# Kernel optimization log

Hardware: AMD Instinct MI355X
Metric: run time of the kernel (lower is better)

Reference implementation:

```python
import jax, jax.numpy as jnp
import numpy as np

M_POS = 0.5
M_NEG_SIM = 0.1
LAM_NEG = 1.0


def setup_inputs() -> dict:
    key = jax.random.key(0)
    N, d, G = 8192, 1024, 64
    codebook = jax.random.normal(key, (N, d), dtype=jnp.float32)
    base = (jnp.arange(N) // G) * G  # contiguous groups of size G (vq_to_range)
    starts = base.astype(jnp.int32)
    ends = (base + G - 1).astype(jnp.int32)
    return {"codebook": codebook, "starts": starts, "ends": ends, "max_i": N - 1}


def reference(codebook, starts, ends, max_i):
    N, d = codebook.shape
    M = min(N, int(max_i) + 1)  # rows processed by the python loop

    # cosine similarity rows [0:M] vs all N
    zn = codebook / jnp.linalg.norm(codebook, axis=-1, keepdims=True)
    cos = jnp.einsum('md,nd->mn', zn[:M], zn)  # (M, N)

    # pairwise Euclidean distances rows [0:M] vs all N via ||a-b||^2 = |a|^2+|b|^2-2ab
    sq = jnp.sum(codebook * codebook, axis=-1)  # (N,)
    dot = jnp.einsum('md,nd->mn', codebook[:M], codebook)  # (M, N)
    d2 = jnp.maximum(sq[:M, None] + sq[None, :] - 2.0 * dot, 0.0)

    j = jnp.arange(N)[None, :]
    i = jnp.arange(M)[:, None]
    in_range = (j >= starts[:M, None]) & (j <= ends[:M, None])
    pos_mask = in_range & (j != i)
    # original: group_mask[i]=False then neg = ~group_mask, so i is in negatives
    neg_mask = (~in_range) | (j == i)

    pos_cnt = jnp.sum(pos_mask, axis=-1)
    neg_cnt = jnp.sum(neg_mask, axis=-1)

    # safe sqrt: only evaluate on positive-mask entries
    D = jnp.sqrt(jnp.where(pos_mask, d2, 1.0))
    pos_term = jnp.square(jax.nn.relu(D - M_POS)) * pos_mask
    pos_pull = jnp.sum(pos_term, axis=-1) / jnp.maximum(pos_cnt, 1)

    neg_cos = jnp.clip(cos, -1.0, 1.0)
    neg_term = jnp.square(jax.nn.relu(jnp.abs(neg_cos) - M_NEG_SIM)) * neg_mask
    ortho = jnp.sum(neg_term, axis=-1) / jnp.maximum(neg_cnt, 1)

    valid = (pos_cnt > 0) & (neg_cnt > 0)
    per_row = jnp.where(valid, pos_pull + LAM_NEG * ortho, 0.0)
    cnt = jnp.sum(valid)
    total = jnp.sum(per_row)
    return jnp.where(cnt > 0, total / jnp.maximum(cnt, 1).astype(total.dtype), jnp.zeros((), total.dtype))
```

## Files before the change

kernel.cpp:

```cpp
#include <hip/hip_runtime.h>
#include <hip/hip_bf16.h>
#include <stdint.h>

#define M_POS 0.5f
#define M_NEG 0.1f
#define LAM_NEG 1.0f

typedef __attribute__((ext_vector_type(4))) float floatx4;
using f8x8 = long;

__global__ __launch_bounds__(256) void prep_kernel(
    const float* __restrict__ cb, unsigned char* __restrict__ cb_q,
    float* __restrict__ sq, float* __restrict__ inv_norm,
    unsigned* __restrict__ zero_base, int zero_len,
    int N, int d)
{
    const int gi = blockIdx.x * 256 + threadIdx.x;
    if (gi < zero_len) zero_base[gi] = 0u;

    const int row = blockIdx.x;
    const float* src = cb + (size_t)row * d;
    unsigned char* dst = cb_q + (size_t)row * d;
    const int t = threadIdx.x;

    float s = 0.f;
    for (int c = t * 4; c < d; c += 1024) {
        float4 v = *(const float4*)(src + c);
        s += v.x * v.x + v.y * v.y + v.z * v.z + v.w * v.w;
        int pk = __builtin_amdgcn_cvt_pk_fp8_f32(v.x, v.y, 0, false);
        pk     = __builtin_amdgcn_cvt_pk_fp8_f32(v.z, v.w, pk, true);
        *(int*)(dst + c) = pk;
    }
    for (int o = 32; o > 0; o >>= 1) s += __shfl_down(s, o, 64);
    __shared__ float wsum[4];
    if ((t & 63) == 0) wsum[t >> 6] = s;
    __syncthreads();
    if (t == 0) {
        float tot = wsum[0] + wsum[1] + wsum[2] + wsum[3];
        sq[row] = tot;
        inv_norm[row] = rsqrtf(tot);
    }
}

__global__ __launch_bounds__(256) void gram_loss_kernel(
    const unsigned char* __restrict__ A,
    const float* __restrict__ sq, const float* __restrict__ inv_norm,
    const int* __restrict__ starts, const int* __restrict__ ends,
    const int* __restrict__ max_ip,
    float* __restrict__ pos_acc, float* __restrict__ neg_acc,
    int N, int d)
{
    const int M = min(N, max_ip[0] + 1);

    const int t = blockIdx.x;
    int bx = (int)((sqrtf(8.f * (float)t + 1.f) - 1.f) * 0.5f);
    while ((bx + 1) * (bx + 2) / 2 <= t) bx++;
    while (bx * (bx + 1) / 2 > t) bx--;
    const int by = t - bx * (bx + 1) / 2;

    const int rowBase = by * 128;
    const int colBase = bx * 128;
    const bool isDiag = (by == bx);

    __shared__ alignas(16) unsigned char ldsA[128 * 64];
    __shared__ alignas(16) unsigned char ldsB[128 * 64];

    const int tid  = threadIdx.x;
    const int wave = tid >> 6;
    const int lane = tid & 63;
    const int wr = (wave >> 1) * 64;
    const int wc = (wave & 1) * 64;

    floatx4 acc[4][4];
#pragma unroll
    for (int a = 0; a < 4; ++a)
#pragma unroll
        for (int b = 0; b < 4; ++b) acc[a][b] = (floatx4){0.f, 0.f, 0.f, 0.f};

    const int sR = lane >> 2;
    const int sQ = lane & 3;
    const int kTiles = d / 64;

    const int rl = lane & 15;
    const int g  = lane >> 4;
    const int rowx = (rl >> 1) & 3;
    const int ghalf = g >> 1;
    const int godd  = (g & 1) * 8;

    for (int kt = 0; kt < kTiles; ++kt) {
        __syncthreads();
        const int k0 = kt * 64;
#pragma unroll
        for (int h = 0; h < 2; ++h) {
            const int r = wave * 32 + h * 16 + sR;
            const int srcQ = sQ ^ ((r >> 1) & 3);
            const unsigned char* ga = A + (size_t)(rowBase + r) * d + k0 + srcQ * 16;
            const unsigned char* gb = A + (size_t)(colBase + r) * d + k0 + srcQ * 16;
            __builtin_amdgcn_global_load_lds(
                (const __attribute__((address_space(1))) void*)ga,
                (__attribute__((address_space(3))) void*)(ldsA + r * 64 + sQ * 16), 16, 0, 0);
            __builtin_amdgcn_global_load_lds(
                (const __attribute__((address_space(1))) void*)gb,
                (__attribute__((address_space(3))) void*)(ldsB + r * 64 + sQ * 16), 16, 0, 0);
        }
        __syncthreads();

#pragma unroll
        for (int ko = 0; ko < 2; ++ko) {
            const int phys16 = ((ko * 2 + ghalf) ^ rowx);
            const int koff = phys16 * 16 + godd;
            f8x8 af[4], bf[4];
#pragma unroll
            for (int t4 = 0; t4 < 4; ++t4) {
                const int ra = wr + t4 * 16 + rl;
                const int rb = wc + t4 * 16 + rl;
                af[t4] = *(const f8x8*)(ldsA + ra * 64 + koff);
                bf[t4] = *(const f8x8*)(ldsB + rb * 64 + koff);
            }
#pragma unroll
            for (int rt = 0; rt < 4; ++rt)
#pragma unroll
                for (int ct = 0; ct < 4; ++ct)
                    acc[rt][ct] = __builtin_amdgcn_mfma_f32_16x16x32_fp8_fp8(
                        af[rt], bf[ct], acc[rt][ct], 0, 0, 0);
        }
    }

    const int q  = lane >> 4;
    const int jlo = colBase + wc;
    const int ilo = rowBase + wr;

    int   jn[4];
    float jinv[4];
    bool  jvalid[4];
#pragma unroll
    for (int ct = 0; ct < 4; ++ct) {
        const int j = jlo + ct * 16 + rl;
        jn[ct]  = j;
        jinv[ct] = inv_norm[j];
        jvalid[ct] = (j < M);
    }

    bool posLane = false;
    {
        const int ri = ilo + lane;
        if (ri < M) posLane |= (ends[ri] >= jlo) && (starts[ri] <= jlo + 63);
        if (!isDiag) {
            const int cj = jlo + lane;
            if (cj < M) posLane |= (ends[cj] >= ilo) && (starts[cj] <= ilo + 63);
        }
    }
    const bool fullPath = (__ballot(posLane) != 0ULL);

    float posc[4] = {0.f, 0.f, 0.f, 0.f};
    float negc[4] = {0.f, 0.f, 0.f, 0.f};

    if (fullPath) {
        int   jns[4], jne[4];
        float jsq[4];
#pragma unroll
        for (int ct = 0; ct < 4; ++ct) {
            jsq[ct] = sq[jn[ct]];
            jns[ct] = jvalid[ct] ? starts[jn[ct]] : 0;
            jne[ct] = jvalid[ct] ? ends[jn[ct]]   : -1;
        }
#pragma unroll
        for (int rt = 0; rt < 4; ++rt) {
            const int ibase = rowBase + wr + rt * 16 + q * 4;
#pragma unroll
            for (int reg = 0; reg < 4; ++reg) {
                const int i = ibase + reg;
                const bool rowValid = (i < M);
                const int ns = rowValid ? starts[i] : 0;
                const int ne = rowValid ? ends[i]   : -1;
                const float iinv = inv_norm[i];
                const float isq  = sq[i];
                float posp = 0.f, negp = 0.f;
#pragma unroll
                for (int ct = 0; ct < 4; ++ct) {
                    const float dot = acc[rt][ct][reg];
                    const int j = jn[ct];
                    float cosv = dot * iinv * jinv[ct];
                    cosv = fminf(fmaxf(cosv, -1.f), 1.f);
                    float tn = fmaxf(fabsf(cosv) - M_NEG, 0.f);
                    const float nterm = tn * tn;
                    const float d2 = fmaxf(isq + jsq[ct] - 2.f * dot, 0.f);
                    float tp = fmaxf(sqrtf(d2) - M_POS, 0.f);
                    const float pterm = tp * tp;
                    const bool dg = (j == i);
                    if (rowValid) {
                        const bool in_r = (j >= ns) && (j <= ne);
                        if (in_r && !dg) posp += pterm;
                        if (!in_r || dg) negp += nterm;
                    }
                    if (!isDiag && jvalid[ct]) {
                        const bool in_c = (i >= jns[ct]) && (i <= jne[ct]);
                        if (in_c && !dg) posc[ct] += pterm;
                        if (!in_c || dg) negc[ct] += nterm;
                    }
                }
#pragma unroll
                for (int m = 1; m < 16; m <<= 1) {
                    posp += __shfl_xor(posp, m, 64);
                    negp += __shfl_xor(negp, m, 64);
                }
                if (rowValid && rl == 0) {
                    atomicAdd(&pos_acc[i], posp);
                    atomicAdd(&neg_acc[i], negp);
                }
            }
        }
        if (!isDiag) {
#pragma unroll
            for (int ct = 0; ct < 4; ++ct) {
                posc[ct] += __shfl_xor(posc[ct], 16, 64);
                posc[ct] += __shfl_xor(posc[ct], 32, 64);
                negc[ct] += __shfl_xor(negc[ct], 16, 64);
                negc[ct] += __shfl_xor(negc[ct], 32, 64);
            }
            if (q == 0) {
#pragma unroll
                for (int ct = 0; ct < 4; ++ct) {
                    if (jvalid[ct]) {
                        atomicAdd(&pos_acc[jn[ct]], posc[ct]);
                        atomicAdd(&neg_acc[jn[ct]], negc[ct]);
                    }
                }
            }
        }
    } else {
#pragma unroll
        for (int rt = 0; rt < 4; ++rt) {
            const int ibase = rowBase + wr + rt * 16 + q * 4;
#pragma unroll
            for (int reg = 0; reg < 4; ++reg) {
                const int i = ibase + reg;
                const float iinv = inv_norm[i];
                float negp = 0.f;
#pragma unroll
                for (int ct = 0; ct < 4; ++ct) {
                    const float dot = acc[rt][ct][reg];
                    float cosv = dot * iinv * jinv[ct];
                    cosv = fminf(fmaxf(cosv, -1.f), 1.f);
                    float tn = fmaxf(fabsf(cosv) - M_NEG, 0.f);
                    const float nterm = tn * tn;
                    negp += nterm;
                    negc[ct] += nterm;
                }
#pragma unroll
                for (int m = 1; m < 16; m <<= 1)
                    negp += __shfl_xor(negp, m, 64);
                if ((i < M) && rl == 0)
                    atomicAdd(&neg_acc[i], negp);
            }
        }
        if (!isDiag) {
#pragma unroll
            for (int ct = 0; ct < 4; ++ct) {
                negc[ct] += __shfl_xor(negc[ct], 16, 64);
                negc[ct] += __shfl_xor(negc[ct], 32, 64);
            }
            if (q == 0) {
#pragma unroll
                for (int ct = 0; ct < 4; ++ct)
                    if (jvalid[ct])
                        atomicAdd(&neg_acc[jn[ct]], negc[ct]);
            }
        }
    }
}

__global__ __launch_bounds__(1024) void finalize_kernel(
    const float* __restrict__ pos_acc, const float* __restrict__ neg_acc,
    const int* __restrict__ starts, const int* __restrict__ ends,
    const int* __restrict__ max_ip, int N, float* __restrict__ out)
{
    const int M = min(N, max_ip[0] + 1);
    const int t = threadIdx.x;
    float total = 0.f;
    int cnt = 0;
    for (int i = t; i < M; i += blockDim.x) {
        const int ns = starts[i], ne = ends[i];
        const int lo = max(ns, 0), hi = min(ne, N - 1);
        const int inr = max(hi - lo + 1, 0);
        const bool dg = (i >= ns) && (i <= ne);
        const int pos_cnt = inr - (dg ? 1 : 0);
        const int neg_cnt = N - inr + (dg ? 1 : 0);
        if (pos_cnt > 0 && neg_cnt > 0) {
            total += pos_acc[i] / (float)max(pos_cnt, 1)
                   + LAM_NEG * neg_acc[i] / (float)max(neg_cnt, 1);
            cnt++;
        }
    }
    for (int o = 32; o > 0; o >>= 1) {
        total += __shfl_down(total, o, 64);
        cnt   += __shfl_down(cnt, o, 64);
    }
    __shared__ float ts[16];
    __shared__ int   cs[16];
    const int w = t >> 6;
    if ((t & 63) == 0) { ts[w] = total; cs[w] = cnt; }
    __syncthreads();
    if (t == 0) {
        float T = 0.f; int C = 0;
        const int nw = blockDim.x >> 6;
        for (int i = 0; i < nw; ++i) { T += ts[i]; C += cs[i]; }
        out[0] = (C > 0) ? T / (float)C : 0.f;
    }
}

extern "C" void kernel_launch(void* const* d_in, const int* in_sizes, int n_in,
                              void* d_out, int out_size, void* d_ws, size_t ws_size,
                              hipStream_t stream) {
    const float* cb     = (const float*)d_in[0];
    const int*   starts = (const int*)d_in[1];
    const int*   ends   = (const int*)d_in[2];
    const int*   max_ip = (const int*)d_in[3];
    float* out = (float*)d_out;

    const int N = in_sizes[1];
    const int d = in_sizes[0] / N;

    char* ws = (char*)d_ws;
    unsigned char* cb_q = (unsigned char*)ws;
    size_t off = ((size_t)N * d + 255) & ~(size_t)255;
    float* sq       = (float*)(ws + off); off += (size_t)N * 4;
    float* inv_norm = (float*)(ws + off); off += (size_t)N * 4;
    float* pos_acc  = (float*)(ws + off); off += (size_t)N * 4;
    float* neg_acc  = (float*)(ws + off); off += (size_t)N * 4;

    prep_kernel<<<N, 256, 0, stream>>>(cb, cb_q, sq, inv_norm,
                                       (unsigned*)pos_acc, 2 * N, N, d);

    const int nb = N / 128;
    const int nBlocks = nb * (nb + 1) / 2;
    gram_loss_kernel<<<nBlocks, 256, 0, stream>>>(cb_q, sq, inv_norm, starts, ends,
                                                  max_ip, pos_acc, neg_acc, N, d);

    finalize_kernel<<<1, 1024, 0, stream>>>(pos_acc, neg_acc, starts, ends, max_ip, N, out);
}
```

Baseline: 213.3 us.

## Double K tile to 128 and fuse finalize into gram kernel via last-block counter

The FP8 Gram kernel now stages 128-wide K slices per iteration with a new XOR swizzle, halving the number of barrier-separated load/compute steps, and declares launch bounds for three blocks per CU. The separate finalize kernel is removed: each block bumps a global counter and the last block reduces the per-row accumulators and writes the output. This saves a kernel launch and sync overhead, at the cost of doubled LDS usage and a serialized tail reduction in one block.

```diff
diff --git a/kernel.cpp b/kernel.cpp
--- a/kernel.cpp
+++ b/kernel.cpp
@@ -42,12 +42,13 @@
     }
 }
 
-__global__ __launch_bounds__(256) void gram_loss_kernel(
+__global__ __launch_bounds__(256, 3) void gram_loss_kernel(
     const unsigned char* __restrict__ A,
     const float* __restrict__ sq, const float* __restrict__ inv_norm,
     const int* __restrict__ starts, const int* __restrict__ ends,
     const int* __restrict__ max_ip,
     float* __restrict__ pos_acc, float* __restrict__ neg_acc,
+    unsigned* __restrict__ counter, float* __restrict__ out,
     int N, int d)
 {
     const int M = min(N, max_ip[0] + 1);
@@ -62,8 +63,8 @@
     const int colBase = bx * 128;
     const bool isDiag = (by == bx);
 
-    __shared__ alignas(16) unsigned char ldsA[128 * 64];
-    __shared__ alignas(16) unsigned char ldsB[128 * 64];
+    __shared__ alignas(16) unsigned char ldsA[128 * 128];
+    __shared__ alignas(16) unsigned char ldsB[128 * 128];
 
     const int tid  = threadIdx.x;
     const int wave = tid >> 6;
@@ -77,45 +78,44 @@
 #pragma unroll
         for (int b = 0; b < 4; ++b) acc[a][b] = (floatx4){0.f, 0.f, 0.f, 0.f};
 
-    const int sR = lane >> 2;
-    const int sQ = lane & 3;
-    const int kTiles = d / 64;
+    const int sRow = lane >> 3;
+    const int sChk = lane & 7;
+    const int srcOffC = ((sChk ^ sRow) * 16);
+    const int kTiles = d / 128;
 
     const int rl = lane & 15;
     const int g  = lane >> 4;
-    const int rowx = (rl >> 1) & 3;
-    const int ghalf = g >> 1;
-    const int godd  = (g & 1) * 8;
+    const int fragOddB = (g & 1) * 8;
+    const int fragChkBase = g >> 1;
+    const int rx = rl & 7;
 
     for (int kt = 0; kt < kTiles; ++kt) {
         __syncthreads();
-        const int k0 = kt * 64;
-#pragma unroll
-        for (int h = 0; h < 2; ++h) {
-            const int r = wave * 32 + h * 16 + sR;
-            const int srcQ = sQ ^ ((r >> 1) & 3);
-            const unsigned char* ga = A + (size_t)(rowBase + r) * d + k0 + srcQ * 16;
-            const unsigned char* gb = A + (size_t)(colBase + r) * d + k0 + srcQ * 16;
+        const int k0 = kt * 128;
+#pragma unroll
+        for (int h = 0; h < 4; ++h) {
+            const int r = wave * 32 + h * 8 + sRow;
+            const unsigned char* ga = A + (size_t)(rowBase + r) * d + k0 + srcOffC;
+            const unsigned char* gb = A + (size_t)(colBase + r) * d + k0 + srcOffC;
             __builtin_amdgcn_global_load_lds(
                 (const __attribute__((address_space(1))) void*)ga,
-                (__attribute__((address_space(3))) void*)(ldsA + r * 64 + sQ * 16), 16, 0, 0);
+                (__attribute__((address_space(3))) void*)(ldsA + r * 128 + sChk * 16), 16, 0, 0);
             __builtin_amdgcn_global_load_lds(
                 (const __attribute__((address_space(1))) void*)gb,
-                (__attribute__((address_space(3))) void*)(ldsB + r * 64 + sQ * 16), 16, 0, 0);
+                (__attribute__((address_space(3))) void*)(ldsB + r * 128 + sChk * 16), 16, 0, 0);
         }
         __syncthreads();
 
 #pragma unroll
-        for (int ko = 0; ko < 2; ++ko) {
-            const int phys16 = ((ko * 2 + ghalf) ^ rowx);
-            const int koff = phys16 * 16 + godd;
+        for (int ko = 0; ko < 4; ++ko) {
+            const int koff = ((2 * ko + fragChkBase) ^ rx) * 16 + fragOddB;
             f8x8 af[4], bf[4];
 #pragma unroll
             for (int t4 = 0; t4 < 4; ++t4) {
                 const int ra = wr + t4 * 16 + rl;
                 const int rb = wc + t4 * 16 + rl;
-                af[t4] = *(const f8x8*)(ldsA + ra * 64 + koff);
-                bf[t4] = *(const f8x8*)(ldsB + rb * 64 + koff);
+                af[t4] = *(const f8x8*)(ldsA + ra * 128 + koff);
+                bf[t4] = *(const f8x8*)(ldsB + rb * 128 + koff);
             }
 #pragma unroll
             for (int rt = 0; rt < 4; ++rt)
@@ -166,7 +166,7 @@
         }
 #pragma unroll
         for (int rt = 0; rt < 4; ++rt) {
-            const int ibase = rowBase + wr + rt * 16 + q * 4;
+            const int ibase = ilo + rt * 16 + q * 4;
 #pragma unroll
             for (int reg = 0; reg < 4; ++reg) {
                 const int i = ibase + reg;
@@ -231,7 +231,7 @@
     } else {
 #pragma unroll
         for (int rt = 0; rt < 4; ++rt) {
-            const int ibase = rowBase + wr + rt * 16 + q * 4;
+            const int ibase = ilo + rt * 16 + q * 4;
 #pragma unroll
             for (int reg = 0; reg < 4; ++reg) {
                 const int i = ibase + reg;
@@ -268,44 +268,47 @@
             }
         }
     }
-}
-
-__global__ __launch_bounds__(1024) void finalize_kernel(
-    const float* __restrict__ pos_acc, const float* __restrict__ neg_acc,
-    const int* __restrict__ starts, const int* __restrict__ ends,
-    const int* __restrict__ max_ip, int N, float* __restrict__ out)
-{
-    const int M = min(N, max_ip[0] + 1);
-    const int t = threadIdx.x;
-    float total = 0.f;
-    int cnt = 0;
-    for (int i = t; i < M; i += blockDim.x) {
-        const int ns = starts[i], ne = ends[i];
-        const int lo = max(ns, 0), hi = min(ne, N - 1);
-        const int inr = max(hi - lo + 1, 0);
-        const bool dg = (i >= ns) && (i <= ne);
-        const int pos_cnt = inr - (dg ? 1 : 0);
-        const int neg_cnt = N - inr + (dg ? 1 : 0);
-        if (pos_cnt > 0 && neg_cnt > 0) {
-            total += pos_acc[i] / (float)max(pos_cnt, 1)
-                   + LAM_NEG * neg_acc[i] / (float)max(neg_cnt, 1);
-            cnt++;
-        }
-    }
-    for (int o = 32; o > 0; o >>= 1) {
-        total += __shfl_down(total, o, 64);
-        cnt   += __shfl_down(cnt, o, 64);
-    }
-    __shared__ float ts[16];
-    __shared__ int   cs[16];
-    const int w = t >> 6;
-    if ((t & 63) == 0) { ts[w] = total; cs[w] = cnt; }
+
+    __shared__ bool amLast;
     __syncthreads();
-    if (t == 0) {
-        float T = 0.f; int C = 0;
-        const int nw = blockDim.x >> 6;
-        for (int i = 0; i < nw; ++i) { T += ts[i]; C += cs[i]; }
-        out[0] = (C > 0) ? T / (float)C : 0.f;
+    if (tid == 0) {
+        __threadfence();
+        unsigned old = atomicAdd(counter, 1u);
+        amLast = (old == (unsigned)(gridDim.x - 1));
+    }
+    __syncthreads();
+    if (amLast) {
+        __threadfence();
+        float total = 0.f;
+        int cnt = 0;
+        for (int i = tid; i < M; i += 256) {
+            const float pa = __hip_atomic_load(&pos_acc[i], __ATOMIC_RELAXED, __HIP_MEMORY_SCOPE_AGENT);
+            const float na = __hip_atomic_load(&neg_acc[i], __ATOMIC_RELAXED, __HIP_MEMORY_SCOPE_AGENT);
+            const int ns = starts[i], ne = ends[i];
+            const int lo = max(ns, 0), hi = min(ne, N - 1);
+            const int inr = max(hi - lo + 1, 0);
+            const bool dg = (i >= ns) && (i <= ne);
+            const int pos_cnt = inr - (dg ? 1 : 0);
+            const int neg_cnt = N - inr + (dg ? 1 : 0);
+            if (pos_cnt > 0 && neg_cnt > 0) {
+                total += pa / (float)max(pos_cnt, 1)
+                       + LAM_NEG * na / (float)max(neg_cnt, 1);
+                cnt++;
+            }
+        }
+        for (int o = 32; o > 0; o >>= 1) {
+            total += __shfl_down(total, o, 64);
+            cnt   += __shfl_down(cnt, o, 64);
+        }
+        __shared__ float fin_ts[4];
+        __shared__ int   fin_cs[4];
+        if ((tid & 63) == 0) { fin_ts[tid >> 6] = total; fin_cs[tid >> 6] = cnt; }
+        __syncthreads();
+        if (tid == 0) {
+            float T = fin_ts[0] + fin_ts[1] + fin_ts[2] + fin_ts[3];
+            int   C = fin_cs[0] + fin_cs[1] + fin_cs[2] + fin_cs[3];
+            out[0] = (C > 0) ? T / (float)C : 0.f;
+        }
     }
 }
 
@@ -328,14 +331,14 @@
     float* inv_norm = (float*)(ws + off); off += (size_t)N * 4;
     float* pos_acc  = (float*)(ws + off); off += (size_t)N * 4;
     float* neg_acc  = (float*)(ws + off); off += (size_t)N * 4;
+    unsigned* counter = (unsigned*)(ws + off); off += 256;
 
     prep_kernel<<<N, 256, 0, stream>>>(cb, cb_q, sq, inv_norm,
-                                       (unsigned*)pos_acc, 2 * N, N, d);
+                                       (unsigned*)pos_acc, 2 * N + 1, N, d);
 
     const int nb = N / 128;
     const int nBlocks = nb * (nb + 1) / 2;
     gram_loss_kernel<<<nBlocks, 256, 0, stream>>>(cb_q, sq, inv_norm, starts, ends,
-                                                  max_ip, pos_acc, neg_acc, N, d);
-
-    finalize_kernel<<<1, 1024, 0, stream>>>(pos_acc, neg_acc, starts, ends, max_ip, N, out);
+                                                  max_ip, pos_acc, neg_acc, counter,
+                                                  out, N, d);
 }
```

After: 213.0 us. Within noise of the previous version (-0.1%).
